# Performance work log

Hardware: AMD Instinct MI355X
Metric: run time of the kernel (lower is better)

## Reference

```python
import jax, jax.numpy as jnp
import numpy as np

D_MODEL = 1024
N_HEAD = 16
D_K = D_MODEL // N_HEAD
NEG = -1e9


def setup_inputs() -> dict:
    key = jax.random.key(0)
    ks = jax.random.split(key, 9)
    B, S = 2, 2048
    scale = 1.0 / np.sqrt(D_MODEL)
    x = jax.random.normal(ks[0], (B, S, D_MODEL), dtype=jnp.float32)
    mask = jnp.tril(jnp.ones((S, S), dtype=jnp.int32))  # causal: 0 => masked
    Wq = jax.random.normal(ks[1], (D_MODEL, D_MODEL), dtype=jnp.float32) * scale
    bq = jnp.zeros((D_MODEL,), dtype=jnp.float32)
    Wk = jax.random.normal(ks[2], (D_MODEL, D_MODEL), dtype=jnp.float32) * scale
    bk = jnp.zeros((D_MODEL,), dtype=jnp.float32)
    Wv = jax.random.normal(ks[3], (D_MODEL, D_MODEL), dtype=jnp.float32) * scale
    bv = jnp.zeros((D_MODEL,), dtype=jnp.float32)
    Wo = jax.random.normal(ks[4], (D_MODEL, D_MODEL), dtype=jnp.float32) * scale
    bo = jnp.zeros((D_MODEL,), dtype=jnp.float32)
    return {"x": x, "mask": mask, "Wq": Wq, "bq": bq, "Wk": Wk, "bk": bk,
            "Wv": Wv, "bv": bv, "Wo": Wo, "bo": bo}


def reference(x, mask, Wq, bq, Wk, bk, Wv, bv, Wo, bo):
    B, S, _ = x.shape
    # torch Linear: y = x @ W.T + b
    def split_heads(y):  # [B,S,D] -> [B,H,S,d_k]
        return y.reshape(B, S, N_HEAD, D_K).transpose(0, 2, 1, 3)
    Q = split_heads(x @ Wq.T + bq)
    K = split_heads(x @ Wk.T + bk)
    V = split_heads(x @ Wv.T + bv)
    scores = jnp.einsum('bhqd,bhkd->bhqk', Q, K) / jnp.sqrt(jnp.float32(D_K))
    scores = jnp.where(mask[None, None, :, :] == 0, jnp.float32(NEG), scores)
    attn = jax.nn.softmax(scores, axis=-1)
    out = jnp.einsum('bhqk,bhkd->bhqd', attn, V)
    out = out.transpose(0, 2, 1, 3).reshape(B, S, D_MODEL)
    return out @ Wo.T + bo
```

## Files before the change

kernel.cpp:

```cpp
#include <hip/hip_runtime.h>
#include <hip/hip_bf16.h>
#include <stdint.h>

#define DM    1024
#define NHEAD 16
#define DKH   64
#define SEQ   2048
#define NB    2
#define MTOT  (NB*SEQ)
#define LSTR  72
#define QSCL  0.18033688f

typedef __hip_bfloat16 bf16;
typedef __attribute__((ext_vector_type(8))) short bf16x8;
typedef __attribute__((ext_vector_type(4))) short bf16x4;
typedef __attribute__((ext_vector_type(4))) float f32x4;

#define MFMA16(a,b,c) __builtin_amdgcn_mfma_f32_16x16x32_bf16((a),(b),(c),0,0,0)

#if __has_builtin(__builtin_amdgcn_exp2f)
#define EXP2F(x) __builtin_amdgcn_exp2f(x)
#else
#define EXP2F(x) __expf(0.69314718056f * (x))
#endif

__device__ __forceinline__ void async_copy16(const void* g, void* l) {
  __builtin_amdgcn_global_load_lds((const __attribute__((address_space(1))) uint32_t*)g,
                                   (__attribute__((address_space(3))) uint32_t*)l,
                                   16, 0, 0);
}

__device__ __forceinline__ short f32_bf16_bits(float f) {
  uint32_t u = __builtin_bit_cast(uint32_t, f);
  u += 0x7FFFu + ((u >> 16) & 1u);
  return (short)(u >> 16);
}

__global__ __launch_bounds__(256) void k_cvt_all(
    const float* __restrict__ x,  const float* __restrict__ Wq,
    const float* __restrict__ Wk, const float* __restrict__ Wv,
    const float* __restrict__ Wo,
    bf16* __restrict__ xb,  bf16* __restrict__ Wqb, bf16* __restrict__ Wkb,
    bf16* __restrict__ Wvb, bf16* __restrict__ Wob) {
  const int NX = (MTOT*DM)/4;
  const int NW = (DM*DM)/4;
  int i = blockIdx.x * 256 + threadIdx.x;
  const float* s; bf16* d; int j; float scl = 1.0f;
  if (i < NX) { s = x; d = xb; j = i; }
  else {
    int t = i - NX;
    int k = t >> 18;
    j = t & (NW - 1);
    s = (k == 0) ? Wq : (k == 1) ? Wk : (k == 2) ? Wv : Wo;
    d = (k == 0) ? Wqb : (k == 1) ? Wkb : (k == 2) ? Wvb : Wob;
    if (k == 0) scl = QSCL;
  }
  float4 v = ((const float4*)s)[j];
  bf16x4 o;
  o[0] = f32_bf16_bits(v.x * scl);
  o[1] = f32_bf16_bits(v.y * scl);
  o[2] = f32_bf16_bits(v.z * scl);
  o[3] = f32_bf16_bits(v.w * scl);
  ((bf16x4*)d)[j] = o;
}

__global__ __launch_bounds__(256) void k_gemm_qkv(
    const bf16* __restrict__ x,
    const bf16* __restrict__ Wq, const bf16* __restrict__ Wk, const bf16* __restrict__ Wv,
    const float* __restrict__ bq, const float* __restrict__ bk, const float* __restrict__ bv,
    bf16* __restrict__ Q, bf16* __restrict__ K, bf16* __restrict__ V) {
  const bf16* W; const float* bias; bf16* C; float bs;
  if (blockIdx.z == 0)      { W = Wq; bias = bq; C = Q; bs = QSCL; }
  else if (blockIdx.z == 1) { W = Wk; bias = bk; C = K; bs = 1.0f; }
  else                      { W = Wv; bias = bv; C = V; bs = 1.0f; }

  __shared__ __align__(16) short As[128*32];
  __shared__ __align__(16) short Bs[128*32];
  const int tid  = threadIdx.x;
  const int lane = tid & 63;
  const int w    = tid >> 6;
  const int wm   = (w & 1) << 6;
  const int wn   = (w >> 1) << 6;
  const int bm   = blockIdx.x << 7;
  const int bn   = blockIdx.y << 7;
  const int m16  = lane & 15;
  const int quad = lane >> 4;
  const int koff = quad << 3;
  const int c0   = (w << 7) | lane;

  f32x4 acc[4][4] = {};

  for (int k0 = 0; k0 < DM; k0 += 32) {
    __syncthreads();
#pragma unroll
    for (int it = 0; it < 2; ++it) {
      int c   = c0 + (it << 6);
      int row = c >> 2;
      int kc  = c & 3;
      async_copy16(x + (size_t)(bm + row) * DM + k0 + (kc << 3),
                   &As[(size_t)((w << 7) + (it << 6)) << 3]);
      async_copy16(W + (size_t)(bn + row) * DM + k0 + (kc << 3),
                   &Bs[(size_t)((w << 7) + (it << 6)) << 3]);
    }
    __syncthreads();

    bf16x8 af[4], bfv[4];
#pragma unroll
    for (int t = 0; t < 4; ++t)
      af[t]  = *(const bf16x8*)&As[(wm + t*16 + m16) * 32 + koff];
#pragma unroll
    for (int t = 0; t < 4; ++t)
      bfv[t] = *(const bf16x8*)&Bs[(wn + t*16 + m16) * 32 + koff];
#pragma unroll
    for (int i = 0; i < 4; ++i)
#pragma unroll
      for (int j = 0; j < 4; ++j)
        acc[i][j] = MFMA16(af[i], bfv[j], acc[i][j]);
  }

  const int crow0 = bm + wm + (quad << 2);
  const int ccol0 = bn + wn + m16;
#pragma unroll
  for (int j = 0; j < 4; ++j) {
    float bv = bias[ccol0 + j*16] * bs;
#pragma unroll
    for (int i = 0; i < 4; ++i)
#pragma unroll
      for (int r = 0; r < 4; ++r)
        C[(size_t)(crow0 + i*16 + r) * DM + ccol0 + j*16] =
            (bf16)(acc[i][j][r] + bv);
  }
}

__global__ __launch_bounds__(256) void k_gemm_o(
    const bf16* __restrict__ A, const bf16* __restrict__ W,
    const float* __restrict__ bias, float* __restrict__ C) {
  __shared__ __align__(16) short As[128*32];
  __shared__ __align__(16) short Bs[64*32];
  const int tid  = threadIdx.x;
  const int lane = tid & 63;
  const int w    = tid >> 6;
  const int wm   = (w & 1) << 6;
  const int wn   = (w >> 1) << 5;
  const int bm   = blockIdx.x << 7;
  const int bn   = blockIdx.y << 6;
  const int m16  = lane & 15;
  const int quad = lane >> 4;
  const int koff = quad << 3;
  const int cA   = (w << 7) | lane;
  const int cB   = (w << 6) | lane;

  f32x4 acc[4][2] = {};

  for (int k0 = 0; k0 < DM; k0 += 32) {
    __syncthreads();
#pragma unroll
    for (int it = 0; it < 2; ++it) {
      int c   = cA + (it << 6);
      int row = c >> 2;
      int kc  = c & 3;
      async_copy16(A + (size_t)(bm + row) * DM + k0 + (kc << 3),
                   &As[(size_t)((w << 7) + (it << 6)) << 3]);
    }
    {
      int row = cB >> 2;
      int kc  = cB & 3;
      async_copy16(W + (size_t)(bn + row) * DM + k0 + (kc << 3),
                   &Bs[(size_t)(w << 6) << 3]);
    }
    __syncthreads();

    bf16x8 af[4], bfv[2];
#pragma unroll
    for (int t = 0; t < 4; ++t)
      af[t]  = *(const bf16x8*)&As[(wm + t*16 + m16) * 32 + koff];
#pragma unroll
    for (int t = 0; t < 2; ++t)
      bfv[t] = *(const bf16x8*)&Bs[(wn + t*16 + m16) * 32 + koff];
#pragma unroll
    for (int i = 0; i < 4; ++i)
#pragma unroll
      for (int j = 0; j < 2; ++j)
        acc[i][j] = MFMA16(af[i], bfv[j], acc[i][j]);
  }

  const int crow0 = bm + wm + (quad << 2);
  const int ccol0 = bn + wn + m16;
#pragma unroll
  for (int j = 0; j < 2; ++j) {
    float bv = bias[ccol0 + j*16];
#pragma unroll
    for (int i = 0; i < 4; ++i)
#pragma unroll
      for (int r = 0; r < 4; ++r)
        C[(size_t)(crow0 + i*16 + r) * DM + ccol0 + j*16] =
            acc[i][j][r] + bv;
  }
}

__global__ __launch_bounds__(256) void k_transpose_v(const bf16* __restrict__ V,
                                                     bf16* __restrict__ Vt) {
  __shared__ __align__(16) short tile[64][LSTR];
  const int tid = threadIdx.x;
  const int s0  = blockIdx.x << 6;
  const int bh  = blockIdx.y;
  const int b   = bh >> 4, h = bh & 15;
#pragma unroll
  for (int it = 0; it < 2; ++it) {
    int c = tid + (it << 8);
    int s = c >> 3, dc = c & 7;
    bf16x8 v = *(const bf16x8*)&V[(size_t)(b*SEQ + s0 + s) * DM + h*DKH + (dc << 3)];
    *(bf16x8*)&tile[s][dc << 3] = v;
  }
  __syncthreads();
#pragma unroll
  for (int it = 0; it < 2; ++it) {
    int c = tid + (it << 8);
    int d = c >> 3, sc = c & 7;
    bf16x8 ov;
#pragma unroll
    for (int i = 0; i < 8; ++i) {
      int p = (sc << 3) + i;
      ov[i] = tile[(p & 3) * 16 + (p >> 2)][d];
    }
    *(bf16x8*)&Vt[((size_t)bh * DKH + d) * SEQ + s0 + (sc << 3)] = ov;
  }
}

__global__ __launch_bounds__(256) void k_attn(const bf16* __restrict__ Q,
                                              const bf16* __restrict__ K,
                                              const bf16* __restrict__ Vt,
                                              bf16* __restrict__ ctx) {
  __shared__ __align__(16) short Ks[64*LSTR];
  __shared__ __align__(16) short Vs[64*LSTR];
  __shared__ __align__(16) short Ps[4][16*LSTR];

  const int tid  = threadIdx.x;
  const int lane = tid & 63;
  const int w    = tid >> 6;
  const int pi   = blockIdx.x;
  const int bh   = blockIdx.y;
  const int b    = bh >> 4, h = bh & 15;
  const int m16  = lane & 15, quad = lane >> 4;
  const int koff = quad << 3;

  const int qt        = (w < 2) ? pi : 63 - pi;
  const int qw        = (qt << 5) + ((w & 1) << 4);
  const int my_ktmax  = qt >> 1;
  const int blk_ktmax = (63 - pi) >> 1;

  const int r0 = tid >> 3, r1 = r0 + 32, c0 = (tid & 7) << 3;

  const bf16* Kb  = K  + (size_t)(b*SEQ) * DM + h*DKH;
  const bf16* Vtb = Vt + (size_t)bh * DKH * SEQ;

  const bf16* Qb = Q + (size_t)(b*SEQ + qw) * DM + h*DKH;
  bf16x8 qf0 = *(const bf16x8*)(Qb + (size_t)m16*DM + koff);
  bf16x8 qf1 = *(const bf16x8*)(Qb + (size_t)m16*DM + 32 + koff);

  f32x4 o[4] = {};
  float ps[4] = {0.f, 0.f, 0.f, 0.f};
  short* Pw = Ps[w];
  const int qg = qw + (quad << 2);

  bf16x8 pk0 = *(const bf16x8*)(Kb  + (size_t)r0*DM + c0);
  bf16x8 pk1 = *(const bf16x8*)(Kb  + (size_t)r1*DM + c0);
  bf16x8 pv0 = *(const bf16x8*)(Vtb + (size_t)r0*SEQ + c0);
  bf16x8 pv1 = *(const bf16x8*)(Vtb + (size_t)r1*SEQ + c0);

  for (int kt = 0; kt <= blk_ktmax; ++kt) {
    __syncthreads();
    *(bf16x8*)&Ks[r0*LSTR + c0] = pk0;
    *(bf16x8*)&Ks[r1*LSTR + c0] = pk1;
    *(bf16x8*)&Vs[r0*LSTR + c0] = pv0;
    *(bf16x8*)&Vs[r1*LSTR + c0] = pv1;
    __syncthreads();

    if (kt < blk_ktmax) {
      const int kn = (kt + 1) << 6;
      pk0 = *(const bf16x8*)(Kb  + (size_t)(kn + r0)*DM + c0);
      pk1 = *(const bf16x8*)(Kb  + (size_t)(kn + r1)*DM + c0);
      pv0 = *(const bf16x8*)(Vtb + (size_t)r0*SEQ + kn + c0);
      pv1 = *(const bf16x8*)(Vtb + (size_t)r1*SEQ + kn + c0);
    }

    if (kt <= my_ktmax) {
      f32x4 sc[4];
#pragma unroll
      for (int st = 0; st < 4; ++st) {
        bf16x8 kf0 = *(const bf16x8*)&Ks[(st*16 + m16)*LSTR + koff];
        bf16x8 kf1 = *(const bf16x8*)&Ks[(st*16 + m16)*LSTR + 32 + koff];
        f32x4 a = {};
        a = MFMA16(qf0, kf0, a);
        a = MFMA16(qf1, kf1, a);
        sc[st] = a;
      }
      const int kk0 = kt << 6;
      if (kt == my_ktmax) {
#pragma unroll
        for (int r = 0; r < 4; ++r) {
          float e[4];
#pragma unroll
          for (int st = 0; st < 4; ++st) {
            float t = EXP2F(sc[st][r]);
            t = (kk0 + st*16 + m16 <= qg + r) ? t : 0.f;
            e[st] = t; ps[r] += t;
          }
          uint32_t lo = (uint16_t)f32_bf16_bits(e[0]) |
                        ((uint32_t)(uint16_t)f32_bf16_bits(e[1]) << 16);
          uint32_t hi = (uint16_t)f32_bf16_bits(e[2]) |
                        ((uint32_t)(uint16_t)f32_bf16_bits(e[3]) << 16);
          *(uint64_t*)&Pw[((quad << 2) + r)*LSTR + (m16 << 2)] =
              (uint64_t)lo | ((uint64_t)hi << 32);
        }
      } else {
#pragma unroll
        for (int r = 0; r < 4; ++r) {
          float e[4];
#pragma unroll
          for (int st = 0; st < 4; ++st) {
            float t = EXP2F(sc[st][r]);
            e[st] = t; ps[r] += t;
          }
          uint32_t lo = (uint16_t)f32_bf16_bits(e[0]) |
                        ((uint32_t)(uint16_t)f32_bf16_bits(e[1]) << 16);
          uint32_t hi = (uint16_t)f32_bf16_bits(e[2]) |
                        ((uint32_t)(uint16_t)f32_bf16_bits(e[3]) << 16);
          *(uint64_t*)&Pw[((quad << 2) + r)*LSTR + (m16 << 2)] =
              (uint64_t)lo | ((uint64_t)hi << 32);
        }
      }
      asm volatile("s_waitcnt lgkmcnt(0)" ::: "memory");
      bf16x8 pa0 = *(const bf16x8*)&Pw[m16*LSTR + koff];
      bf16x8 pa1 = *(const bf16x8*)&Pw[m16*LSTR + 32 + koff];
#pragma unroll
      for (int t = 0; t < 4; ++t) {
        bf16x8 vf0 = *(const bf16x8*)&Vs[(t*16 + m16)*LSTR + koff];
        bf16x8 vf1 = *(const bf16x8*)&Vs[(t*16 + m16)*LSTR + 32 + koff];
        o[t] = MFMA16(pa0, vf0, o[t]);
        o[t] = MFMA16(pa1, vf1, o[t]);
      }
    }
  }

  bf16* Cb = ctx + (size_t)(b*SEQ + qw) * DM + h*DKH;
#pragma unroll
  for (int r = 0; r < 4; ++r) {
    float v = ps[r];
    v += __shfl_xor(v, 1, 64);
    v += __shfl_xor(v, 2, 64);
    v += __shfl_xor(v, 4, 64);
    v += __shfl_xor(v, 8, 64);
    float inv = 1.0f / v;
#pragma unroll
    for (int t = 0; t < 4; ++t)
      Cb[(size_t)((quad << 2) + r) * DM + t*16 + m16] = (bf16)(o[t][r] * inv);
  }
}

extern "C" void kernel_launch(void* const* d_in, const int* in_sizes, int n_in,
                              void* d_out, int out_size, void* d_ws, size_t ws_size,
                              hipStream_t stream) {
  const float* x  = (const float*)d_in[0];
  const float* Wq = (const float*)d_in[2];
  const float* bq = (const float*)d_in[3];
  const float* Wk = (const float*)d_in[4];
  const float* bk = (const float*)d_in[5];
  const float* Wv = (const float*)d_in[6];
  const float* bv = (const float*)d_in[7];
  const float* Wo = (const float*)d_in[8];
  const float* bo = (const float*)d_in[9];
  float* out = (float*)d_out;

  const size_t SZ = (size_t)MTOT * DM;
  const size_t WZ = (size_t)DM * DM;
  bf16* xb  = (bf16*)d_ws;
  bf16* Wqb = xb  + SZ;
  bf16* Wkb = Wqb + WZ;
  bf16* Wvb = Wkb + WZ;
  bf16* Wob = Wvb + WZ;
  bf16* Qb  = Wob + WZ;
  bf16* Kb  = Qb  + SZ;
  bf16* Vb  = Kb  + SZ;
  bf16* Vtb = Vb  + SZ;
  bf16* Cx  = xb;

  k_cvt_all<<<(SZ/4 + 4*(WZ/4))/256, 256, 0, stream>>>(
      x, Wq, Wk, Wv, Wo, xb, Wqb, Wkb, Wvb, Wob);

  k_gemm_qkv<<<dim3(MTOT/128, DM/128, 3), 256, 0, stream>>>(
      xb, Wqb, Wkb, Wvb, bq, bk, bv, Qb, Kb, Vb);
  k_transpose_v<<<dim3(SEQ/64, NB*NHEAD), 256, 0, stream>>>(Vb, Vtb);
  k_attn<<<dim3(32, NB*NHEAD), 256, 0, stream>>>(Qb, Kb, Vtb, Cx);
  k_gemm_o<<<dim3(MTOT/128, DM/64), 256, 0, stream>>>(Cx, Wob, bo, out);
}
```

Before: 202.1 us.

## Have each attention wave process both paired causal q-tiles sequentially with 128-thread blocks

Attention blocks shrink from four waves to two, and each wave now processes a 16-row slice of both the short and long causal query tiles in two phases. This removes waves that idle while waiting on the longer tile's loop. In exchange, each K/V tile is shared by fewer waves, which increases global and LDS load traffic per unit of compute. Each wave also holds two sets of accumulators, which raises register use.

```diff
diff --git a/kernel.cpp b/kernel.cpp
--- a/kernel.cpp
+++ b/kernel.cpp
@@ -227,13 +227,13 @@
   }
 }
 
-__global__ __launch_bounds__(256) void k_attn(const bf16* __restrict__ Q,
+__global__ __launch_bounds__(128) void k_attn(const bf16* __restrict__ Q,
                                               const bf16* __restrict__ K,
                                               const bf16* __restrict__ Vt,
                                               bf16* __restrict__ ctx) {
   __shared__ __align__(16) short Ks[64*LSTR];
   __shared__ __align__(16) short Vs[64*LSTR];
-  __shared__ __align__(16) short Ps[4][16*LSTR];
+  __shared__ __align__(16) short Ps[2][16*LSTR];
 
   const int tid  = threadIdx.x;
   const int lane = tid & 63;
@@ -244,117 +244,119 @@
   const int m16  = lane & 15, quad = lane >> 4;
   const int koff = quad << 3;
 
-  const int qt        = (w < 2) ? pi : 63 - pi;
-  const int qw        = (qt << 5) + ((w & 1) << 4);
-  const int my_ktmax  = qt >> 1;
-  const int blk_ktmax = (63 - pi) >> 1;
-
-  const int r0 = tid >> 3, r1 = r0 + 32, c0 = (tid & 7) << 3;
+  const int qa = pi, qb = 63 - pi;
+  const int ktA = qa >> 1, ktB = qb >> 1;
+  const int NIT = ktA + ktB + 2;
+
+  const int r0 = tid >> 3, c0 = (tid & 7) << 3;
 
   const bf16* Kb  = K  + (size_t)(b*SEQ) * DM + h*DKH;
   const bf16* Vtb = Vt + (size_t)bh * DKH * SEQ;
 
-  const bf16* Qb = Q + (size_t)(b*SEQ + qw) * DM + h*DKH;
-  bf16x8 qf0 = *(const bf16x8*)(Qb + (size_t)m16*DM + koff);
-  bf16x8 qf1 = *(const bf16x8*)(Qb + (size_t)m16*DM + 32 + koff);
-
-  f32x4 o[4] = {};
-  float ps[4] = {0.f, 0.f, 0.f, 0.f};
+  const int qwA = (qa << 5) + (w << 4);
+  const int qwB = (qb << 5) + (w << 4);
+  const bf16* QbA = Q + (size_t)(b*SEQ + qwA) * DM + h*DKH;
+  const bf16* QbB = Q + (size_t)(b*SEQ + qwB) * DM + h*DKH;
+  bf16x8 qfA0 = *(const bf16x8*)(QbA + (size_t)m16*DM + koff);
+  bf16x8 qfA1 = *(const bf16x8*)(QbA + (size_t)m16*DM + 32 + koff);
+  bf16x8 qfB0 = *(const bf16x8*)(QbB + (size_t)m16*DM + koff);
+  bf16x8 qfB1 = *(const bf16x8*)(QbB + (size_t)m16*DM + 32 + koff);
+
+  f32x4 oA[4] = {}, oB[4] = {};
+  float psA[4] = {0.f,0.f,0.f,0.f}, psB[4] = {0.f,0.f,0.f,0.f};
   short* Pw = Ps[w];
-  const int qg = qw + (quad << 2);
-
-  bf16x8 pk0 = *(const bf16x8*)(Kb  + (size_t)r0*DM + c0);
-  bf16x8 pk1 = *(const bf16x8*)(Kb  + (size_t)r1*DM + c0);
-  bf16x8 pv0 = *(const bf16x8*)(Vtb + (size_t)r0*SEQ + c0);
-  bf16x8 pv1 = *(const bf16x8*)(Vtb + (size_t)r1*SEQ + c0);
-
-  for (int kt = 0; kt <= blk_ktmax; ++kt) {
-    __syncthreads();
-    *(bf16x8*)&Ks[r0*LSTR + c0] = pk0;
-    *(bf16x8*)&Ks[r1*LSTR + c0] = pk1;
-    *(bf16x8*)&Vs[r0*LSTR + c0] = pv0;
-    *(bf16x8*)&Vs[r1*LSTR + c0] = pv1;
-    __syncthreads();
-
-    if (kt < blk_ktmax) {
-      const int kn = (kt + 1) << 6;
-      pk0 = *(const bf16x8*)(Kb  + (size_t)(kn + r0)*DM + c0);
-      pk1 = *(const bf16x8*)(Kb  + (size_t)(kn + r1)*DM + c0);
-      pv0 = *(const bf16x8*)(Vtb + (size_t)r0*SEQ + kn + c0);
-      pv1 = *(const bf16x8*)(Vtb + (size_t)r1*SEQ + kn + c0);
-    }
-
-    if (kt <= my_ktmax) {
-      f32x4 sc[4];
+  const int qgA = qwA + (quad << 2);
+  const int qgB = qwB + (quad << 2);
+
+  auto work = [&](f32x4* o, float* ps, bf16x8 qf0, bf16x8 qf1,
+                  int qg, int kk0, bool diag) {
+    f32x4 sc[4];
+#pragma unroll
+    for (int st = 0; st < 4; ++st) {
+      bf16x8 kf0 = *(const bf16x8*)&Ks[(st*16 + m16)*LSTR + koff];
+      bf16x8 kf1 = *(const bf16x8*)&Ks[(st*16 + m16)*LSTR + 32 + koff];
+      f32x4 a = {};
+      a = MFMA16(qf0, kf0, a);
+      a = MFMA16(qf1, kf1, a);
+      sc[st] = a;
+    }
+#pragma unroll
+    for (int r = 0; r < 4; ++r) {
+      float e[4];
 #pragma unroll
       for (int st = 0; st < 4; ++st) {
-        bf16x8 kf0 = *(const bf16x8*)&Ks[(st*16 + m16)*LSTR + koff];
-        bf16x8 kf1 = *(const bf16x8*)&Ks[(st*16 + m16)*LSTR + 32 + koff];
-        f32x4 a = {};
-        a = MFMA16(qf0, kf0, a);
-        a = MFMA16(qf1, kf1, a);
-        sc[st] = a;
+        float t = EXP2F(sc[st][r]);
+        if (diag) t = (kk0 + st*16 + m16 <= qg + r) ? t : 0.f;
+        e[st] = t; ps[r] += t;
       }
-      const int kk0 = kt << 6;
-      if (kt == my_ktmax) {
-#pragma unroll
-        for (int r = 0; r < 4; ++r) {
-          float e[4];
-#pragma unroll
-          for (int st = 0; st < 4; ++st) {
-            float t = EXP2F(sc[st][r]);
-            t = (kk0 + st*16 + m16 <= qg + r) ? t : 0.f;
-            e[st] = t; ps[r] += t;
-          }
-          uint32_t lo = (uint16_t)f32_bf16_bits(e[0]) |
-                        ((uint32_t)(uint16_t)f32_bf16_bits(e[1]) << 16);
-          uint32_t hi = (uint16_t)f32_bf16_bits(e[2]) |
-                        ((uint32_t)(uint16_t)f32_bf16_bits(e[3]) << 16);
-          *(uint64_t*)&Pw[((quad << 2) + r)*LSTR + (m16 << 2)] =
-              (uint64_t)lo | ((uint64_t)hi << 32);
-        }
-      } else {
-#pragma unroll
-        for (int r = 0; r < 4; ++r) {
-          float e[4];
-#pragma unroll
-          for (int st = 0; st < 4; ++st) {
-            float t = EXP2F(sc[st][r]);
-            e[st] = t; ps[r] += t;
-          }
-          uint32_t lo = (uint16_t)f32_bf16_bits(e[0]) |
-                        ((uint32_t)(uint16_t)f32_bf16_bits(e[1]) << 16);
-          uint32_t hi = (uint16_t)f32_bf16_bits(e[2]) |
-                        ((uint32_t)(uint16_t)f32_bf16_bits(e[3]) << 16);
-          *(uint64_t*)&Pw[((quad << 2) + r)*LSTR + (m16 << 2)] =
-              (uint64_t)lo | ((uint64_t)hi << 32);
-        }
+      uint32_t lo = (uint16_t)f32_bf16_bits(e[0]) |
+                    ((uint32_t)(uint16_t)f32_bf16_bits(e[1]) << 16);
+      uint32_t hi = (uint16_t)f32_bf16_bits(e[2]) |
+                    ((uint32_t)(uint16_t)f32_bf16_bits(e[3]) << 16);
+      *(uint64_t*)&Pw[((quad << 2) + r)*LSTR + (m16 << 2)] =
+          (uint64_t)lo | ((uint64_t)hi << 32);
+    }
+    asm volatile("s_waitcnt lgkmcnt(0)" ::: "memory");
+    bf16x8 pa0 = *(const bf16x8*)&Pw[m16*LSTR + koff];
+    bf16x8 pa1 = *(const bf16x8*)&Pw[m16*LSTR + 32 + koff];
+#pragma unroll
+    for (int t = 0; t < 4; ++t) {
+      bf16x8 vf0 = *(const bf16x8*)&Vs[(t*16 + m16)*LSTR + koff];
+      bf16x8 vf1 = *(const bf16x8*)&Vs[(t*16 + m16)*LSTR + 32 + koff];
+      o[t] = MFMA16(pa0, vf0, o[t]);
+      o[t] = MFMA16(pa1, vf1, o[t]);
+    }
+  };
+
+  bf16x8 pk[4], pv[4];
+#pragma unroll
+  for (int j = 0; j < 4; ++j) {
+    pk[j] = *(const bf16x8*)(Kb  + (size_t)(r0 + 16*j)*DM + c0);
+    pv[j] = *(const bf16x8*)(Vtb + (size_t)(r0 + 16*j)*SEQ + c0);
+  }
+
+  for (int i = 0; i < NIT; ++i) {
+    const bool phB = i > ktA;
+    const int  kt  = phB ? i - ktA - 1 : i;
+    __syncthreads();
+#pragma unroll
+    for (int j = 0; j < 4; ++j) {
+      *(bf16x8*)&Ks[(r0 + 16*j)*LSTR + c0] = pk[j];
+      *(bf16x8*)&Vs[(r0 + 16*j)*LSTR + c0] = pv[j];
+    }
+    __syncthreads();
+
+    if (i + 1 < NIT) {
+      const bool nB = (i + 1) > ktA;
+      const int  nk = nB ? i - ktA : i + 1;
+      const int  nb = nk << 6;
+#pragma unroll
+      for (int j = 0; j < 4; ++j) {
+        pk[j] = *(const bf16x8*)(Kb  + (size_t)(nb + r0 + 16*j)*DM + c0);
+        pv[j] = *(const bf16x8*)(Vtb + (size_t)(r0 + 16*j)*SEQ + nb + c0);
       }
-      asm volatile("s_waitcnt lgkmcnt(0)" ::: "memory");
-      bf16x8 pa0 = *(const bf16x8*)&Pw[m16*LSTR + koff];
-      bf16x8 pa1 = *(const bf16x8*)&Pw[m16*LSTR + 32 + koff];
-#pragma unroll
-      for (int t = 0; t < 4; ++t) {
-        bf16x8 vf0 = *(const bf16x8*)&Vs[(t*16 + m16)*LSTR + koff];
-        bf16x8 vf1 = *(const bf16x8*)&Vs[(t*16 + m16)*LSTR + 32 + koff];
-        o[t] = MFMA16(pa0, vf0, o[t]);
-        o[t] = MFMA16(pa1, vf1, o[t]);
-      }
-    }
-  }
-
-  bf16* Cb = ctx + (size_t)(b*SEQ + qw) * DM + h*DKH;
+    }
+
+    const int kk0 = kt << 6;
+    if (phB) work(oB, psB, qfB0, qfB1, qgB, kk0, kt == ktB);
+    else     work(oA, psA, qfA0, qfA1, qgA, kk0, kt == ktA);
+  }
+
+  bf16* CbA = ctx + (size_t)(b*SEQ + qwA) * DM + h*DKH;
+  bf16* CbB = ctx + (size_t)(b*SEQ + qwB) * DM + h*DKH;
 #pragma unroll
   for (int r = 0; r < 4; ++r) {
-    float v = ps[r];
-    v += __shfl_xor(v, 1, 64);
-    v += __shfl_xor(v, 2, 64);
-    v += __shfl_xor(v, 4, 64);
-    v += __shfl_xor(v, 8, 64);
-    float inv = 1.0f / v;
-#pragma unroll
-    for (int t = 0; t < 4; ++t)
-      Cb[(size_t)((quad << 2) + r) * DM + t*16 + m16] = (bf16)(o[t][r] * inv);
+    float va = psA[r], vb = psB[r];
+    va += __shfl_xor(va, 1, 64); vb += __shfl_xor(vb, 1, 64);
+    va += __shfl_xor(va, 2, 64); vb += __shfl_xor(vb, 2, 64);
+    va += __shfl_xor(va, 4, 64); vb += __shfl_xor(vb, 4, 64);
+    va += __shfl_xor(va, 8, 64); vb += __shfl_xor(vb, 8, 64);
+    float ia = 1.0f / va, ib = 1.0f / vb;
+#pragma unroll
+    for (int t = 0; t < 4; ++t) {
+      CbA[(size_t)((quad << 2) + r) * DM + t*16 + m16] = (bf16)(oA[t][r] * ia);
+      CbB[(size_t)((quad << 2) + r) * DM + t*16 + m16] = (bf16)(oB[t][r] * ib);
+    }
   }
 }
 
@@ -391,6 +393,6 @@
   k_gemm_qkv<<<dim3(MTOT/128, DM/128, 3), 256, 0, stream>>>(
       xb, Wqb, Wkb, Wvb, bq, bk, bv, Qb, Kb, Vb);
   k_transpose_v<<<dim3(SEQ/64, NB*NHEAD), 256, 0, stream>>>(Vb, Vtb);
-  k_attn<<<dim3(32, NB*NHEAD), 256, 0, stream>>>(Qb, Kb, Vtb, Cx);
+  k_attn<<<dim3(32, NB*NHEAD), 128, 0, stream>>>(Qb, Kb, Vtb, Cx);
   k_gemm_o<<<dim3(MTOT/128, DM/64), 256, 0, stream>>>(Cx, Wob, bo, out);
 }
```

After: 229.6 us. 13.6% more time.

## Use single-wave attention blocks reading K/V directly from global memory

Applied to the files above, without the earlier changes.

The attention kernel changes from 256-thread blocks that share K/V tiles through LDS with double-buffered prefetch and block-wide barriers to 64-thread single-wave blocks, one per 16-query strip. K and V fragments are loaded straight from global memory into MFMA operands. Blocks are ordered heaviest-first to balance the causal workload. This removes the barriers and the LDS staging and gives many more independent blocks, but each wave now reloads K/V with no reuse across waves and the loads are no longer prefetched, so it leans on L2/L1 bandwidth and latency hiding through occupancy.

```diff
diff --git a/kernel.cpp b/kernel.cpp
--- a/kernel.cpp
+++ b/kernel.cpp
@@ -227,29 +227,21 @@
   }
 }
 
-__global__ __launch_bounds__(256) void k_attn(const bf16* __restrict__ Q,
-                                              const bf16* __restrict__ K,
-                                              const bf16* __restrict__ Vt,
-                                              bf16* __restrict__ ctx) {
-  __shared__ __align__(16) short Ks[64*LSTR];
-  __shared__ __align__(16) short Vs[64*LSTR];
-  __shared__ __align__(16) short Ps[4][16*LSTR];
-
-  const int tid  = threadIdx.x;
-  const int lane = tid & 63;
-  const int w    = tid >> 6;
-  const int pi   = blockIdx.x;
-  const int bh   = blockIdx.y;
-  const int b    = bh >> 4, h = bh & 15;
+__global__ __launch_bounds__(64) void k_attn(const bf16* __restrict__ Q,
+                                             const bf16* __restrict__ K,
+                                             const bf16* __restrict__ Vt,
+                                             bf16* __restrict__ ctx) {
+  __shared__ __align__(16) short Pw[16*LSTR];
+
+  const int lane = threadIdx.x;
   const int m16  = lane & 15, quad = lane >> 4;
   const int koff = quad << 3;
-
-  const int qt        = (w < 2) ? pi : 63 - pi;
-  const int qw        = (qt << 5) + ((w & 1) << 4);
-  const int my_ktmax  = qt >> 1;
-  const int blk_ktmax = (63 - pi) >> 1;
-
-  const int r0 = tid >> 3, r1 = r0 + 32, c0 = (tid & 7) << 3;
+  const int i    = blockIdx.x;
+  const int bh   = i & 31;
+  const int b    = bh >> 4, h = bh & 15;
+  const int sb   = 127 - (i >> 5);
+  const int qw   = sb << 4;
+  const int ktmax = sb >> 2;
 
   const bf16* Kb  = K  + (size_t)(b*SEQ) * DM + h*DKH;
   const bf16* Vtb = Vt + (size_t)bh * DKH * SEQ;
@@ -260,86 +252,65 @@
 
   f32x4 o[4] = {};
   float ps[4] = {0.f, 0.f, 0.f, 0.f};
-  short* Pw = Ps[w];
   const int qg = qw + (quad << 2);
 
-  bf16x8 pk0 = *(const bf16x8*)(Kb  + (size_t)r0*DM + c0);
-  bf16x8 pk1 = *(const bf16x8*)(Kb  + (size_t)r1*DM + c0);
-  bf16x8 pv0 = *(const bf16x8*)(Vtb + (size_t)r0*SEQ + c0);
-  bf16x8 pv1 = *(const bf16x8*)(Vtb + (size_t)r1*SEQ + c0);
-
-  for (int kt = 0; kt <= blk_ktmax; ++kt) {
-    __syncthreads();
-    *(bf16x8*)&Ks[r0*LSTR + c0] = pk0;
-    *(bf16x8*)&Ks[r1*LSTR + c0] = pk1;
-    *(bf16x8*)&Vs[r0*LSTR + c0] = pv0;
-    *(bf16x8*)&Vs[r1*LSTR + c0] = pv1;
-    __syncthreads();
-
-    if (kt < blk_ktmax) {
-      const int kn = (kt + 1) << 6;
-      pk0 = *(const bf16x8*)(Kb  + (size_t)(kn + r0)*DM + c0);
-      pk1 = *(const bf16x8*)(Kb  + (size_t)(kn + r1)*DM + c0);
-      pv0 = *(const bf16x8*)(Vtb + (size_t)r0*SEQ + kn + c0);
-      pv1 = *(const bf16x8*)(Vtb + (size_t)r1*SEQ + kn + c0);
-    }
-
-    if (kt <= my_ktmax) {
-      f32x4 sc[4];
-#pragma unroll
-      for (int st = 0; st < 4; ++st) {
-        bf16x8 kf0 = *(const bf16x8*)&Ks[(st*16 + m16)*LSTR + koff];
-        bf16x8 kf1 = *(const bf16x8*)&Ks[(st*16 + m16)*LSTR + 32 + koff];
-        f32x4 a = {};
-        a = MFMA16(qf0, kf0, a);
-        a = MFMA16(qf1, kf1, a);
-        sc[st] = a;
+  for (int kt = 0; kt <= ktmax; ++kt) {
+    const int kk0 = kt << 6;
+    f32x4 sc[4];
+#pragma unroll
+    for (int st = 0; st < 4; ++st) {
+      const bf16* kr = Kb + (size_t)(kk0 + st*16 + m16) * DM;
+      bf16x8 kf0 = *(const bf16x8*)(kr + koff);
+      bf16x8 kf1 = *(const bf16x8*)(kr + 32 + koff);
+      f32x4 a = {};
+      a = MFMA16(qf0, kf0, a);
+      a = MFMA16(qf1, kf1, a);
+      sc[st] = a;
+    }
+    if (kt == ktmax) {
+#pragma unroll
+      for (int r = 0; r < 4; ++r) {
+        float e[4];
+#pragma unroll
+        for (int st = 0; st < 4; ++st) {
+          float t = EXP2F(sc[st][r]);
+          t = (kk0 + st*16 + m16 <= qg + r) ? t : 0.f;
+          e[st] = t; ps[r] += t;
+        }
+        uint32_t lo = (uint16_t)f32_bf16_bits(e[0]) |
+                      ((uint32_t)(uint16_t)f32_bf16_bits(e[1]) << 16);
+        uint32_t hi = (uint16_t)f32_bf16_bits(e[2]) |
+                      ((uint32_t)(uint16_t)f32_bf16_bits(e[3]) << 16);
+        *(uint64_t*)&Pw[((quad << 2) + r)*LSTR + (m16 << 2)] =
+            (uint64_t)lo | ((uint64_t)hi << 32);
       }
-      const int kk0 = kt << 6;
-      if (kt == my_ktmax) {
-#pragma unroll
-        for (int r = 0; r < 4; ++r) {
-          float e[4];
-#pragma unroll
-          for (int st = 0; st < 4; ++st) {
-            float t = EXP2F(sc[st][r]);
-            t = (kk0 + st*16 + m16 <= qg + r) ? t : 0.f;
-            e[st] = t; ps[r] += t;
-          }
-          uint32_t lo = (uint16_t)f32_bf16_bits(e[0]) |
-                        ((uint32_t)(uint16_t)f32_bf16_bits(e[1]) << 16);
-          uint32_t hi = (uint16_t)f32_bf16_bits(e[2]) |
-                        ((uint32_t)(uint16_t)f32_bf16_bits(e[3]) << 16);
-          *(uint64_t*)&Pw[((quad << 2) + r)*LSTR + (m16 << 2)] =
-              (uint64_t)lo | ((uint64_t)hi << 32);
+    } else {
+#pragma unroll
+      for (int r = 0; r < 4; ++r) {
+        float e[4];
+#pragma unroll
+        for (int st = 0; st < 4; ++st) {
+          float t = EXP2F(sc[st][r]);
+          e[st] = t; ps[r] += t;
         }
-      } else {
-#pragma unroll
-        for (int r = 0; r < 4; ++r) {
-          float e[4];
-#pragma unroll
-          for (int st = 0; st < 4; ++st) {
-            float t = EXP2F(sc[st][r]);
-            e[st] = t; ps[r] += t;
-          }
-          uint32_t lo = (uint16_t)f32_bf16_bits(e[0]) |
-                        ((uint32_t)(uint16_t)f32_bf16_bits(e[1]) << 16);
-          uint32_t hi = (uint16_t)f32_bf16_bits(e[2]) |
-                        ((uint32_t)(uint16_t)f32_bf16_bits(e[3]) << 16);
-          *(uint64_t*)&Pw[((quad << 2) + r)*LSTR + (m16 << 2)] =
-              (uint64_t)lo | ((uint64_t)hi << 32);
-        }
+        uint32_t lo = (uint16_t)f32_bf16_bits(e[0]) |
+                      ((uint32_t)(uint16_t)f32_bf16_bits(e[1]) << 16);
+        uint32_t hi = (uint16_t)f32_bf16_bits(e[2]) |
+                      ((uint32_t)(uint16_t)f32_bf16_bits(e[3]) << 16);
+        *(uint64_t*)&Pw[((quad << 2) + r)*LSTR + (m16 << 2)] =
+            (uint64_t)lo | ((uint64_t)hi << 32);
       }
-      asm volatile("s_waitcnt lgkmcnt(0)" ::: "memory");
-      bf16x8 pa0 = *(const bf16x8*)&Pw[m16*LSTR + koff];
-      bf16x8 pa1 = *(const bf16x8*)&Pw[m16*LSTR + 32 + koff];
-#pragma unroll
-      for (int t = 0; t < 4; ++t) {
-        bf16x8 vf0 = *(const bf16x8*)&Vs[(t*16 + m16)*LSTR + koff];
-        bf16x8 vf1 = *(const bf16x8*)&Vs[(t*16 + m16)*LSTR + 32 + koff];
-        o[t] = MFMA16(pa0, vf0, o[t]);
-        o[t] = MFMA16(pa1, vf1, o[t]);
-      }
+    }
+    asm volatile("s_waitcnt lgkmcnt(0)" ::: "memory");
+    bf16x8 pa0 = *(const bf16x8*)&Pw[m16*LSTR + koff];
+    bf16x8 pa1 = *(const bf16x8*)&Pw[m16*LSTR + 32 + koff];
+#pragma unroll
+    for (int t = 0; t < 4; ++t) {
+      const bf16* vr = Vtb + (size_t)(t*16 + m16) * SEQ + kk0;
+      bf16x8 vf0 = *(const bf16x8*)(vr + koff);
+      bf16x8 vf1 = *(const bf16x8*)(vr + 32 + koff);
+      o[t] = MFMA16(pa0, vf0, o[t]);
+      o[t] = MFMA16(pa1, vf1, o[t]);
     }
   }
 
@@ -391,6 +362,6 @@
   k_gemm_qkv<<<dim3(MTOT/128, DM/128, 3), 256, 0, stream>>>(
       xb, Wqb, Wkb, Wvb, bq, bk, bv, Qb, Kb, Vb);
   k_transpose_v<<<dim3(SEQ/64, NB*NHEAD), 256, 0, stream>>>(Vb, Vtb);
-  k_attn<<<dim3(32, NB*NHEAD), 256, 0, stream>>>(Qb, Kb, Vtb, Cx);
+  k_attn<<<dim3(4096), 64, 0, stream>>>(Qb, Kb, Vtb, Cx);
   k_gemm_o<<<dim3(MTOT/128, DM/64), 256, 0, stream>>>(Cx, Wob, bo, out);
 }
```

New measurement: 282.6 us. +39.8%, slower.
